# Optimization experiments

Measured on AMD Instinct MI355X. Metric: run time of the kernel, lower is better.

## Reference

```python
import jax, jax.numpy as jnp
import numpy as np

B, T, D, NH, V, L = 2, 1024, 1024, 16, 32000, 4  # L = blocks * layers_per_block
HD = D // NH
FF = 4 * D


def rmsnorm(x, gamma, beta):
    # matches RMSNorm: mean of squares over last dim (tp pmean is identity on 1 device)
    ms = jnp.mean(jnp.square(x), axis=-1, keepdims=True)
    return (x / jnp.sqrt(ms + 1e-6)) * gamma + beta


def setup_inputs() -> dict:
    key = jax.random.key(0)
    ks = jax.random.split(key, 16)
    s = 0.02
    inp = {
        "tokens": jax.random.randint(ks[0], (B, T), 0, V, dtype=jnp.int32),
        "emb_W": jax.random.normal(ks[1], (V, D), jnp.float32) * s,
        "pos_W": jax.random.normal(ks[2], (T, D), jnp.float32) * s,
        "g1": jnp.ones((L, D), jnp.float32),
        "be1": jnp.zeros((L, D), jnp.float32),
        "Wqkv": jax.random.normal(ks[3], (L, D, 3 * D), jnp.float32) * s,
        "bqkv": jnp.zeros((L, 3 * D), jnp.float32),
        "Wo": jax.random.normal(ks[4], (L, D, D), jnp.float32) * s,
        "bo": jnp.zeros((L, D), jnp.float32),
        "g2": jnp.ones((L, D), jnp.float32),
        "be2": jnp.zeros((L, D), jnp.float32),
        "Wf1": jax.random.normal(ks[5], (L, D, FF), jnp.float32) * s,
        "bf1": jnp.zeros((L, FF), jnp.float32),
        "Wf2": jax.random.normal(ks[6], (L, FF, D), jnp.float32) * s,
        "bf2": jnp.zeros((L, D), jnp.float32),
        "gf": jnp.ones((D,), jnp.float32),
        "bef": jnp.zeros((D,), jnp.float32),
    }
    return inp


def _forward(tokens, emb_W, pos_W, g1, be1, Wqkv, bqkv, Wo, bo, g2, be2,
             Wf1, bf1, Wf2, bf2, gf, bef):
    x = emb_W[tokens] + pos_W[jnp.arange(T)]  # [B, T, D]
    causal = jnp.tril(jnp.ones((T, T), dtype=bool))
    scale = HD ** -0.5
    for i in range(L):
        # attention sub-block
        h = rmsnorm(x, g1[i], be1[i])
        qkv = h @ Wqkv[i] + bqkv[i]
        q, k, v = jnp.split(qkv, 3, axis=-1)
        q = q.reshape(B, T, NH, HD).transpose(0, 2, 1, 3)  # B nh T d
        k = k.reshape(B, T, NH, HD).transpose(0, 2, 1, 3)
        v = v.reshape(B, T, NH, HD).transpose(0, 2, 1, 3)
        att = jnp.einsum('bhqd,bhkd->bhqk', q, k) * scale
        att = jnp.where(causal, att, -jnp.inf)
        att = jax.nn.softmax(att, axis=-1)
        o = jnp.einsum('bhqk,bhkd->bhqd', att, v)
        o = o.transpose(0, 2, 1, 3).reshape(B, T, D)
        x = x + (o @ Wo[i] + bo[i])
        # FFN sub-block (selu, dropout off since train=False)
        h = rmsnorm(x, g2[i], be2[i])
        f = jax.nn.selu(h @ Wf1[i] + bf1[i]) @ Wf2[i] + bf2[i]
        x = x + f
    # tied output head: final RMSNorm then embedding.attend
    x = rmsnorm(x, gf, bef)
    logits = jnp.einsum('btd,vd->btv', x, emb_W)
    return logits


def reference(tokens, emb_W, pos_W, g1, be1, Wqkv, bqkv, Wo, bo, g2, be2,
              Wf1, bf1, Wf2, bf2, gf, bef):
    return _forward(tokens, emb_W, pos_W, g1, be1, Wqkv, bqkv, Wo, bo,
                    g2, be2, Wf1, bf1, Wf2, bf2, gf, bef)
```

## Files before the change

kernel.cpp:

```cpp
#include <hip/hip_runtime.h>

typedef unsigned short u16;
typedef __attribute__((ext_vector_type(8))) short bf16x8;
typedef __attribute__((ext_vector_type(4))) float f32x4;

#define DD 1024
#define TT 1024
#define NHH 16
#define VV 32000
#define FFF 4096
#define LL 4
#define MM 2048
#define TD3 3072

__device__ __forceinline__ u16 f2bfu(float f) {
  unsigned int x = __builtin_bit_cast(unsigned int, f);
  return (u16)((x + 0x7FFFu + ((x >> 16) & 1u)) >> 16);
}

__device__ __forceinline__ void gl16(const u16* g, u16* l) {
  __builtin_amdgcn_global_load_lds((const __attribute__((address_space(1))) void*)g,
                                   (__attribute__((address_space(3))) void*)l, 16, 0, 0);
}

template <int N>
__device__ __forceinline__ void vwait() {
  if constexpr (N == 0) asm volatile("s_waitcnt vmcnt(0)" ::: "memory");
  else if constexpr (N == 4) asm volatile("s_waitcnt vmcnt(4)" ::: "memory");
  else asm volatile("s_waitcnt vmcnt(8)" ::: "memory");
}

__global__ void transpose_cvt_k(const float* __restrict__ in, u16* __restrict__ out,
                                int K, int N) {
  const size_t mat = (size_t)K * N;
  in += (size_t)blockIdx.z * mat;
  out += (size_t)blockIdx.z * mat;
  __shared__ float tile[32][33];
  const int n0 = blockIdx.x << 5, k0 = blockIdx.y << 5;
  const int tx = threadIdx.x, ty = threadIdx.y;
#pragma unroll
  for (int i = 0; i < 32; i += 8) tile[ty + i][tx] = in[(size_t)(k0 + ty + i) * N + n0 + tx];
  __syncthreads();
#pragma unroll
  for (int i = 0; i < 32; i += 8)
    out[(size_t)(n0 + ty + i) * K + k0 + tx] = f2bfu(tile[tx][ty + i]);
}

__global__ void cvt_bf16_k(const float* __restrict__ in, u16* __restrict__ out, long n4) {
  const long i = (long)blockIdx.x * blockDim.x + threadIdx.x;
  if (i >= n4) return;
  const float4 v = ((const float4*)in)[i];
  ushort4 o;
  o.x = f2bfu(v.x); o.y = f2bfu(v.y); o.z = f2bfu(v.z); o.w = f2bfu(v.w);
  ((ushort4*)out)[i] = o;
}

__global__ void embed_k(const int* __restrict__ tok, const float* __restrict__ emb,
                        const float* __restrict__ pos, float* __restrict__ x) {
  const int m = blockIdx.x, tid = threadIdx.x;
  const int t = m & (TT - 1);
  const int id = tok[m];
  const float4 e = ((const float4*)(emb + (size_t)id * DD))[tid];
  const float4 p = ((const float4*)(pos + (size_t)t * DD))[tid];
  float4 r;
  r.x = e.x + p.x; r.y = e.y + p.y; r.z = e.z + p.z; r.w = e.w + p.w;
  ((float4*)(x + (size_t)m * DD))[tid] = r;
}

__global__ void rmsnorm_k(const float* __restrict__ x, const float* __restrict__ g,
                          const float* __restrict__ be, u16* __restrict__ out) {
  const int row = blockIdx.x, tid = threadIdx.x;
  const float4 xv = ((const float4*)(x + (size_t)row * DD))[tid];
  float ss = xv.x * xv.x + xv.y * xv.y + xv.z * xv.z + xv.w * xv.w;
#pragma unroll
  for (int o = 32; o; o >>= 1) ss += __shfl_xor(ss, o);
  __shared__ float sm[4];
  if ((tid & 63) == 0) sm[tid >> 6] = ss;
  __syncthreads();
  const float tot = sm[0] + sm[1] + sm[2] + sm[3];
  const float rs = rsqrtf(tot * (1.f / DD) + 1e-6f);
  const float4 gv = ((const float4*)g)[tid];
  const float4 bv = ((const float4*)be)[tid];
  ushort4 o4;
  o4.x = f2bfu(xv.x * rs * gv.x + bv.x);
  o4.y = f2bfu(xv.y * rs * gv.y + bv.y);
  o4.z = f2bfu(xv.z * rs * gv.z + bv.z);
  o4.w = f2bfu(xv.w * rs * gv.w + bv.w);
  ((ushort4*)(out + (size_t)row * DD))[tid] = o4;
}

template <int NP>
__global__ void addres_rms_k(float* __restrict__ x, const float* __restrict__ pp,
                             const float* __restrict__ bias, const float* __restrict__ g,
                             const float* __restrict__ be, u16* __restrict__ out) {
  const int row = blockIdx.x, tid = threadIdx.x;
  const size_t base = (size_t)row * (DD / 4) + tid;
  float4 s = ((float4*)x)[base];
  const float4 bv = ((const float4*)bias)[tid];
  s.x += bv.x; s.y += bv.y; s.z += bv.z; s.w += bv.w;
#pragma unroll
  for (int p = 0; p < NP; ++p) {
    const float4 pv = ((const float4*)pp)[(size_t)p * (MM * DD / 4) + base];
    s.x += pv.x; s.y += pv.y; s.z += pv.z; s.w += pv.w;
  }
  ((float4*)x)[base] = s;
  float ss = s.x * s.x + s.y * s.y + s.z * s.z + s.w * s.w;
#pragma unroll
  for (int o = 32; o; o >>= 1) ss += __shfl_xor(ss, o);
  __shared__ float sm[4];
  if ((tid & 63) == 0) sm[tid >> 6] = ss;
  __syncthreads();
  const float tot = sm[0] + sm[1] + sm[2] + sm[3];
  const float rs = rsqrtf(tot * (1.f / DD) + 1e-6f);
  const float4 gv = ((const float4*)g)[tid];
  const float4 bev = ((const float4*)be)[tid];
  ushort4 o4;
  o4.x = f2bfu(s.x * rs * gv.x + bev.x);
  o4.y = f2bfu(s.y * rs * gv.y + bev.y);
  o4.z = f2bfu(s.z * rs * gv.z + bev.z);
  o4.w = f2bfu(s.w * rs * gv.w + bev.w);
  ((ushort4*)(out + (size_t)row * DD))[tid] = o4;
}

__global__ void pack_vt_k(const u16* __restrict__ qkv, u16* __restrict__ Vt) {
  const int z = blockIdx.x;
  const int t0 = blockIdx.y << 6;
  const int b = z >> 4, h = z & 15;
  __shared__ u16 tile[64][72];
  const int tid = threadIdx.x;
  for (int c = tid; c < 512; c += 256) {
    const int t = c >> 3, d8 = (c & 7) << 3;
    union { uint4 u; u16 s[8]; } tmp;
    tmp.u = *(const uint4*)(qkv + (long)(b * TT + t0 + t) * TD3 + 2 * DD + h * 64 + d8);
#pragma unroll
    for (int j = 0; j < 8; ++j) tile[d8 + j][t] = tmp.s[j];
  }
  __syncthreads();
  for (int c = tid; c < 512; c += 256) {
    const int d = c >> 3, t8 = (c & 7) << 3;
    *(uint4*)(Vt + ((long)z * 64 + d) * TT + t0 + t8) = *(const uint4*)&tile[d][t8];
  }
}

__global__ __launch_bounds__(256) void flash_k(const u16* __restrict__ qkv,
                                               const u16* __restrict__ Vt,
                                               u16* __restrict__ o) {
  const int z = blockIdx.x;
  const int pair = blockIdx.y;
  const int b = z >> 4, h = z & 15;
  const int tid = threadIdx.x;
  const int lane = tid & 63;
  const int w = tid >> 6;

  __shared__ u16 Qs[64 * 64];
  __shared__ u16 Ks[128 * 64];
  __shared__ u16 Vs[64 * 128];
  __shared__ u16 Ps[64 * 128];

  const u16* qbase = qkv + (size_t)b * TT * TD3;
  const int kcb = (lane >> 4) << 4;

  for (int half = 0; half < 2; ++half) {
    const int qa = half ? (15 - pair) : pair;
    const int q0 = qa << 6;
    const int nkt = (qa >> 1) + 1;

#pragma unroll
    for (int c = 0; c < 2; ++c) {
      const int rbase = c * 32 + w * 8;
      const int row = rbase + (lane >> 3);
      const u16* src = qbase + (long)(q0 + row) * TD3 + h * 64 +
                       ((((lane & 7) << 4) ^ ((row & 7) << 4)) >> 1);
      gl16(src, &Qs[rbase * 64]);
    }

    float m_r[4], l_r[4];
    f32x4 oacc[4];
#pragma unroll
    for (int r = 0; r < 4; ++r) { m_r[r] = -1e30f; l_r[r] = 0.f; }
#pragma unroll
    for (int nd = 0; nd < 4; ++nd) oacc[nd] = (f32x4){0.f, 0.f, 0.f, 0.f};

    for (int kt = 0; kt < nkt; ++kt) {
      const int t0 = kt << 7;
#pragma unroll
      for (int c = 0; c < 4; ++c) {
        const int rbase = c * 32 + w * 8;
        const int row = rbase + (lane >> 3);
        const u16* src = qbase + (long)(t0 + row) * TD3 + DD + h * 64 +
                         ((((lane & 7) << 4) ^ ((row & 7) << 4)) >> 1);
        gl16(src, &Ks[rbase * 64]);
      }
#pragma unroll
      for (int c = 0; c < 4; ++c) {
        const int rbase = c * 16 + w * 4;
        const int d = rbase + (lane >> 4);
        const u16* src = Vt + ((long)(z * 64 + d)) * TT + t0 +
                         ((((lane & 15) << 4) ^ ((d & 7) << 4)) >> 1);
        gl16(src, &Vs[rbase * 128]);
      }
      __syncthreads();

      f32x4 sacc[8];
#pragma unroll
      for (int ni = 0; ni < 8; ++ni) sacc[ni] = (f32x4){0.f, 0.f, 0.f, 0.f};
      const int qrow = (w << 4) + (lane & 15);
#pragma unroll
      for (int ks = 0; ks < 2; ++ks) {
        const bf16x8 aq = *(const bf16x8*)&Qs[qrow * 64 + (((ks * 64 + kcb) ^ ((qrow & 7) << 4)) >> 1)];
#pragma unroll
        for (int ni = 0; ni < 8; ++ni) {
          const int key = (lane & 15) + (ni << 4);
          const bf16x8 bk = *(const bf16x8*)&Ks[key * 64 + (((ks * 64 + kcb) ^ ((key & 7) << 4)) >> 1)];
          sacc[ni] = __builtin_amdgcn_mfma_f32_16x16x32_bf16(aq, bk, sacc[ni], 0, 0, 0);
        }
      }

      float mx[4] = {-1e30f, -1e30f, -1e30f, -1e30f};
      const bool diag = (kt == nkt - 1);
#pragma unroll
      for (int ni = 0; ni < 8; ++ni)
#pragma unroll
        for (int r = 0; r < 4; ++r) {
          float v = sacc[ni][r] * 0.125f;
          if (diag) {
            const int key = t0 + (lane & 15) + (ni << 4);
            const int qq = q0 + (w << 4) + ((lane >> 4) << 2) + r;
            if (key > qq) v = -1e30f;
          }
          sacc[ni][r] = v;
          mx[r] = fmaxf(mx[r], v);
        }
#pragma unroll
      for (int st = 1; st < 16; st <<= 1)
#pragma unroll
        for (int r = 0; r < 4; ++r) mx[r] = fmaxf(mx[r], __shfl_xor(mx[r], st));
      float sc[4], sum[4];
#pragma unroll
      for (int r = 0; r < 4; ++r) {
        const float mn = fmaxf(m_r[r], mx[r]);
        sc[r] = __expf(m_r[r] - mn);
        m_r[r] = mn;
        sum[r] = 0.f;
      }
#pragma unroll
      for (int ni = 0; ni < 8; ++ni)
#pragma unroll
        for (int r = 0; r < 4; ++r) {
          const float e = __expf(sacc[ni][r] - m_r[r]);
          sum[r] += e;
          const int prow = (w << 4) + ((lane >> 4) << 2) + r;
          const int pcol = (lane & 15) + (ni << 4);
          Ps[prow * 128 + (((pcol << 1) ^ ((prow & 7) << 4)) >> 1)] = f2bfu(e);
        }
#pragma unroll
      for (int st = 1; st < 16; st <<= 1)
#pragma unroll
        for (int r = 0; r < 4; ++r) sum[r] += __shfl_xor(sum[r], st);
#pragma unroll
      for (int r = 0; r < 4; ++r) l_r[r] = l_r[r] * sc[r] + sum[r];
#pragma unroll
      for (int nd = 0; nd < 4; ++nd)
#pragma unroll
        for (int r = 0; r < 4; ++r) oacc[nd][r] *= sc[r];

#pragma unroll
      for (int ks2 = 0; ks2 < 4; ++ks2) {
        const int prow = (w << 4) + (lane & 15);
        const bf16x8 pa = *(const bf16x8*)&Ps[prow * 128 + (((ks2 * 64 + kcb) ^ ((prow & 7) << 4)) >> 1)];
#pragma unroll
        for (int nd = 0; nd < 4; ++nd) {
          const int dd2 = (lane & 15) + (nd << 4);
          const bf16x8 vb = *(const bf16x8*)&Vs[dd2 * 128 + (((ks2 * 64 + kcb) ^ ((dd2 & 7) << 4)) >> 1)];
          oacc[nd] = __builtin_amdgcn_mfma_f32_16x16x32_bf16(pa, vb, oacc[nd], 0, 0, 0);
        }
      }
      __syncthreads();
    }

    float inv[4];
#pragma unroll
    for (int r = 0; r < 4; ++r) inv[r] = 1.f / l_r[r];
#pragma unroll
    for (int nd = 0; nd < 4; ++nd)
#pragma unroll
      for (int r = 0; r < 4; ++r) {
        const int row = q0 + (w << 4) + ((lane >> 4) << 2) + r;
        const int col = (h << 6) + (lane & 15) + (nd << 4);
        o[(long)(b * TT + row) * DD + col] = f2bfu(oacc[nd][r] * inv[r]);
      }
  }
}

enum { EPI_BF16 = 0, EPI_BF16_BIAS = 1, EPI_SELU = 2, EPI_F32 = 3, EPI_RESID = 4 };

template <int EPI>
__global__ __launch_bounds__(256) void gemm_bt(
    const u16* __restrict__ A, long az1, long az2, int lda,
    const u16* __restrict__ Bt, long bz1, long bz2, int ldb,
    void* __restrict__ C, long cz1, long cz2, int ldc,
    const float* __restrict__ bias, int Nvalid, int K) {
  const int z = blockIdx.z;
  A += (long)(z >> 4) * az1 + (long)(z & 15) * az2;
  Bt += (long)(z >> 4) * bz1 + (long)(z & 15) * bz2;
  const long coff = (long)(z >> 4) * cz1 + (long)(z & 15) * cz2;

  __shared__ u16 ldsA[2][128 * 32];
  __shared__ u16 ldsB[2][128 * 32];

  const int tid = threadIdx.x;
  const int lane = tid & 63;
  const int wave = tid >> 6;
  const int wr = wave >> 1, wc = wave & 1;
  const int m0 = blockIdx.x << 7, n0 = blockIdx.y << 7;

  f32x4 acc[4][4];
#pragma unroll
  for (int i = 0; i < 4; ++i)
#pragma unroll
    for (int j = 0; j < 4; ++j) acc[i][j] = (f32x4){0.f, 0.f, 0.f, 0.f};

  auto STAGE = [&](int buf, int kt) {
    const int k0 = kt << 5;
#pragma unroll
    for (int p = 0; p < 2; ++p) {
      const int c = tid + (p << 8);
      const int row = c >> 2, col = (c & 3) << 3;
      gl16(A + (long)(m0 + row) * lda + k0 + col, &ldsA[buf][c << 3]);
      gl16(Bt + (long)(n0 + row) * ldb + k0 + col, &ldsB[buf][c << 3]);
    }
  };

  const int nk = K >> 5;
  STAGE(0, 0);
  __syncthreads();
  int cur = 0;
  for (int kt = 0; kt < nk; ++kt) {
    if (kt + 1 < nk) STAGE(cur ^ 1, kt + 1);
    const int rb = lane & 15;
    const int kc = (lane >> 4) << 3;
    bf16x8 af[4], bfr[4];
#pragma unroll
    for (int mi = 0; mi < 4; ++mi)
      af[mi] = *(const bf16x8*)&ldsA[cur][(((wr << 6) + (mi << 4) + rb) << 5) + kc];
#pragma unroll
    for (int ni = 0; ni < 4; ++ni)
      bfr[ni] = *(const bf16x8*)&ldsB[cur][(((wc << 6) + (ni << 4) + rb) << 5) + kc];
#pragma unroll
    for (int mi = 0; mi < 4; ++mi)
#pragma unroll
      for (int ni = 0; ni < 4; ++ni)
        acc[mi][ni] = __builtin_amdgcn_mfma_f32_16x16x32_bf16(af[mi], bfr[ni], acc[mi][ni], 0, 0, 0);
    __syncthreads();
    cur ^= 1;
  }

  const int row0 = m0 + (wr << 6) + ((lane >> 4) << 2);
  const int col0 = n0 + (wc << 6) + (lane & 15);
#pragma unroll
  for (int ni = 0; ni < 4; ++ni) {
    const int col = col0 + (ni << 4);
    if (col >= Nvalid) continue;
    float bv = 0.f;
    if (EPI == EPI_BF16_BIAS || EPI == EPI_SELU || EPI == EPI_RESID) bv = bias[col];
#pragma unroll
    for (int mi = 0; mi < 4; ++mi) {
#pragma unroll
      for (int r = 0; r < 4; ++r) {
        const int row = row0 + (mi << 4) + r;
        const long idx = coff + (long)row * ldc + col;
        float v = acc[mi][ni][r] + bv;
        if (EPI == EPI_SELU)
          v = v > 0.f ? 1.0507009873554805f * v : 1.7580993408473766f * (__expf(v) - 1.f);
        if (EPI == EPI_BF16 || EPI == EPI_BF16_BIAS || EPI == EPI_SELU)
          ((u16*)C)[idx] = f2bfu(v);
        else if (EPI == EPI_F32)
          ((float*)C)[idx] = v;
        else
          ((float*)C)[idx] += v;
      }
    }
  }
}

template <int EPI>
__global__ __launch_bounds__(256) void gemm_bt3(
    const u16* __restrict__ A, long az1, long az2, int lda,
    const u16* __restrict__ Bt, long bz1, long bz2, int ldb,
    void* __restrict__ C, long cz1, long cz2, int ldc,
    const float* __restrict__ bias, int Nvalid, int K) {
  const int z = blockIdx.z;
  A += (long)(z >> 4) * az1 + (long)(z & 15) * az2;
  Bt += (long)(z >> 4) * bz1 + (long)(z & 15) * bz2;
  const long coff = (long)(z >> 4) * cz1 + (long)(z & 15) * cz2;

  __shared__ u16 ldsA[3][128 * 32];
  __shared__ u16 ldsB[3][128 * 32];

  const int tid = threadIdx.x;
  const int lane = tid & 63;
  const int wave = tid >> 6;
  const int wr = wave >> 1, wc = wave & 1;
  const int m0 = blockIdx.x << 7, n0 = blockIdx.y << 7;

  f32x4 acc[4][4];
#pragma unroll
  for (int i = 0; i < 4; ++i)
#pragma unroll
    for (int j = 0; j < 4; ++j) acc[i][j] = (f32x4){0.f, 0.f, 0.f, 0.f};

  auto STAGE = [&](int buf, int kt) {
    const int k0 = kt << 5;
#pragma unroll
    for (int p = 0; p < 2; ++p) {
      const int c = tid + (p << 8);
      const int row = c >> 2, col = (c & 3) << 3;
      gl16(A + (long)(m0 + row) * lda + k0 + col, &ldsA[buf][c << 3]);
      gl16(Bt + (long)(n0 + row) * ldb + k0 + col, &ldsB[buf][c << 3]);
    }
  };

  const int nk = K >> 5;
  STAGE(0, 0);
  STAGE(1, 1);

  const int rb = lane & 15;
  const int kc = (lane >> 4) << 3;
  int cur = 0, stg = 2;
#pragma unroll 1
  for (int kt = 0; kt < nk; ++kt) {
    if (kt + 1 < nk) vwait<4>();
    else vwait<0>();
    __builtin_amdgcn_s_barrier();
    __builtin_amdgcn_sched_barrier(0);

    bf16x8 af[4], bfr[4];
#pragma unroll
    for (int mi = 0; mi < 4; ++mi)
      af[mi] = *(const bf16x8*)&ldsA[cur][(((wr << 6) + (mi << 4) + rb) << 5) + kc];
#pragma unroll
    for (int ni = 0; ni < 4; ++ni)
      bfr[ni] = *(const bf16x8*)&ldsB[cur][(((wc << 6) + (ni << 4) + rb) << 5) + kc];
    asm volatile("s_waitcnt lgkmcnt(0)" ::: "memory");
    __builtin_amdgcn_sched_barrier(0);
    __builtin_amdgcn_s_barrier();
    __builtin_amdgcn_sched_barrier(0);
    if (kt + 2 < nk) STAGE(stg, kt + 2);
    __builtin_amdgcn_sched_barrier(0);

    __builtin_amdgcn_s_setprio(1);
#pragma unroll
    for (int mi = 0; mi < 4; ++mi)
#pragma unroll
      for (int ni = 0; ni < 4; ++ni)
        acc[mi][ni] = __builtin_amdgcn_mfma_f32_16x16x32_bf16(af[mi], bfr[ni], acc[mi][ni], 0, 0, 0);
    __builtin_amdgcn_s_setprio(0);

    cur = (cur == 2) ? 0 : cur + 1;
    stg = (stg == 2) ? 0 : stg + 1;
  }

  const int row0 = m0 + (wr << 6) + ((lane >> 4) << 2);
  const int col0 = n0 + (wc << 6) + (lane & 15);
#pragma unroll
  for (int ni = 0; ni < 4; ++ni) {
    const int col = col0 + (ni << 4);
    if (col >= Nvalid) continue;
    float bv = 0.f;
    if (EPI == EPI_BF16_BIAS || EPI == EPI_SELU || EPI == EPI_RESID) bv = bias[col];
#pragma unroll
    for (int mi = 0; mi < 4; ++mi) {
#pragma unroll
      for (int r = 0; r < 4; ++r) {
        const int row = row0 + (mi << 4) + r;
        const long idx = coff + (long)row * ldc + col;
        float v = acc[mi][ni][r] + bv;
        if (EPI == EPI_SELU)
          v = v > 0.f ? 1.0507009873554805f * v : 1.7580993408473766f * (__expf(v) - 1.f);
        if (EPI == EPI_BF16 || EPI == EPI_BF16_BIAS || EPI == EPI_SELU)
          ((u16*)C)[idx] = f2bfu(v);
        else if (EPI == EPI_F32)
          ((float*)C)[idx] = v;
        else
          ((float*)C)[idx] += v;
      }
    }
  }
}

template <int KDIM>
__global__ __launch_bounds__(512) void gemm256_k(
    const u16* __restrict__ A, int lda,
    const u16* __restrict__ Bt, int ldb,
    float* __restrict__ C, int ldc, int mm) {
  extern __shared__ u16 smem[];
  u16* SA = smem;
  u16* SB = smem + 24576;

  const int nwg = gridDim.x;
  const int q = nwg >> 3, r = nwg & 7;
  const int xcd = blockIdx.x & 7, loc = blockIdx.x >> 3;
  const int wg = (xcd < r) ? (xcd * (q + 1) + loc) : (r * (q + 1) + (xcd - r) * q + loc);
  const int m0 = (wg % mm) << 8;
  const int n0 = (wg / mm) << 8;

  const int tid = threadIdx.x;
  const int lane = tid & 63;
  const int w = tid >> 6;
  const int wr = w >> 2, wc = w & 3;
  const int l = lane & 15, kq = lane >> 4;

  f32x4 acc[8][4];
#pragma unroll
  for (int i = 0; i < 8; ++i)
#pragma unroll
    for (int j = 0; j < 4; ++j) acc[i][j] = (f32x4){0.f, 0.f, 0.f, 0.f};

  auto STAGE = [&](int p, int kt) {
    u16* la = SA + (p << 13);
    u16* lb = SB + (p << 13);
    const int k0 = kt << 5;
#pragma unroll
    for (int hh = 0; hh < 2; ++hh) {
      const int c = tid + (hh << 9);
      const int r2 = c >> 3, sp = c & 7;
      const int s = sp ^ (r2 & 7);
      const int row = r2 + ((s >> 2) << 7);
      const int col = k0 + ((s & 3) << 3);
      gl16(A + (size_t)(m0 + row) * lda + col, la + (c << 3));
      gl16(Bt + (size_t)(n0 + row) * ldb + col, lb + (c << 3));
    }
  };

  constexpr int NK = KDIM >> 5;
  STAGE(0, 0);
  STAGE(1, 1);
  STAGE(2, 2);

  int buf = 0;
#pragma unroll 1
  for (int t = 0; t < NK; ++t) {
    if (t + 2 < NK) vwait<8>();
    else if (t + 1 < NK) vwait<4>();
    else vwait<0>();
    __builtin_amdgcn_s_barrier();
    __builtin_amdgcn_sched_barrier(0);

    const u16* a = SA + (buf << 13);
    const u16* b = SB + (buf << 13);
    auto rdA = [&](int mi) -> bf16x8 {
      const int row = (wr << 7) + (mi << 4) + l;
      const int r2 = row & 127;
      const int sp = (((row >> 7) << 2) + kq) ^ (r2 & 7);
      return *(const bf16x8*)&a[(r2 << 6) + (sp << 3)];
    };
    auto rdB = [&](int ni) -> bf16x8 {
      const int row = (wc << 6) + (ni << 4) + l;
      const int r2 = row & 127;
      const int sp = (((row >> 7) << 2) + kq) ^ (r2 & 7);
      return *(const bf16x8*)&b[(r2 << 6) + (sp << 3)];
    };

    bf16x8 af[8], bfr[4];
#pragma unroll
    for (int ni = 0; ni < 4; ++ni) bfr[ni] = rdB(ni);
#pragma unroll
    for (int mi = 0; mi < 8; ++mi) af[mi] = rdA(mi);
    asm volatile("s_waitcnt lgkmcnt(0)" ::: "memory");
    __builtin_amdgcn_sched_barrier(0);
    __builtin_amdgcn_s_barrier();
    __builtin_amdgcn_sched_barrier(0);
    if (t + 3 < NK) STAGE(buf, t + 3);
    __builtin_amdgcn_sched_barrier(0);

    __builtin_amdgcn_s_setprio(1);
#pragma unroll
    for (int mi = 0; mi < 8; ++mi)
#pragma unroll
      for (int ni = 0; ni < 4; ++ni)
        acc[mi][ni] = __builtin_amdgcn_mfma_f32_16x16x32_bf16(af[mi], bfr[ni], acc[mi][ni], 0, 0, 0);
    __builtin_amdgcn_s_setprio(0);
    buf = (buf == 2) ? 0 : buf + 1;
  }

  float* lf = (float*)smem + (size_t)w * 1088;
#pragma unroll 1
  for (int mi = 0; mi < 8; ++mi) {
    asm volatile("s_waitcnt lgkmcnt(0)" ::: "memory");
    __builtin_amdgcn_sched_barrier(0);
#pragma unroll
    for (int ni = 0; ni < 4; ++ni)
#pragma unroll
      for (int rr = 0; rr < 4; ++rr)
        lf[((kq << 2) + rr) * 68 + (ni << 4) + l] = acc[mi][ni][rr];
    asm volatile("s_waitcnt lgkmcnt(0)" ::: "memory");
    __builtin_amdgcn_sched_barrier(0);
#pragma unroll
    for (int p = 0; p < 4; ++p) {
      const int rl = (p << 2) + kq;
      const f32x4 v = *(const f32x4*)&lf[rl * 68 + (l << 2)];
      const int row = m0 + (wr << 7) + (mi << 4) + rl;
      const int col = n0 + (wc << 6) + (l << 2);
      *(f32x4*)(C + (size_t)row * ldc + col) = v;
    }
  }
}

extern "C" void kernel_launch(void* const* d_in, const int* in_sizes, int n_in,
                              void* d_out, int out_size, void* d_ws, size_t ws_size,
                              hipStream_t stream) {
  const int* tokens = (const int*)d_in[0];
  const float* emb_W = (const float*)d_in[1];
  const float* pos_W = (const float*)d_in[2];
  const float* g1 = (const float*)d_in[3];
  const float* be1 = (const float*)d_in[4];
  const float* Wqkv = (const float*)d_in[5];
  const float* bqkv = (const float*)d_in[6];
  const float* Wo = (const float*)d_in[7];
  const float* bo = (const float*)d_in[8];
  const float* g2 = (const float*)d_in[9];
  const float* be2 = (const float*)d_in[10];
  const float* Wf1 = (const float*)d_in[11];
  const float* bf1 = (const float*)d_in[12];
  const float* Wf2 = (const float*)d_in[13];
  const float* bf2 = (const float*)d_in[14];
  const float* gf = (const float*)d_in[15];
  const float* bef = (const float*)d_in[16];

  char* w = (char*)d_ws;
  auto alloc = [&](size_t bytes) {
    char* p = w;
    w += (bytes + 255) & ~(size_t)255;
    return p;
  };
  u16* WqkvT = (u16*)alloc((size_t)LL * TD3 * DD * 2);
  u16* WoT   = (u16*)alloc((size_t)LL * DD * DD * 2);
  u16* Wf1T  = (u16*)alloc((size_t)LL * FFF * DD * 2);
  u16* Wf2T  = (u16*)alloc((size_t)LL * DD * FFF * 2);
  u16* embB  = (u16*)alloc((size_t)VV * DD * 2);
  float* x   = (float*)alloc((size_t)MM * DD * 4);
  u16* h     = (u16*)alloc((size_t)MM * DD * 2);
  u16* qkv   = (u16*)alloc((size_t)MM * TD3 * 2);
  u16* Vt    = (u16*)alloc((size_t)32 * 64 * TT * 2);
  u16* o     = (u16*)alloc((size_t)MM * DD * 2);
  u16* h1    = (u16*)alloc((size_t)MM * FFF * 2);
  float* pp  = (float*)alloc((size_t)4 * MM * DD * 4);

  bool big =
      hipFuncSetAttribute((const void*)&gemm256_k<1024>,
                          hipFuncAttributeMaxDynamicSharedMemorySize, 98304) == hipSuccess;

  dim3 tb(32, 8);
  transpose_cvt_k<<<dim3(TD3 / 32, DD / 32, LL), tb, 0, stream>>>(Wqkv, WqkvT, DD, TD3);
  transpose_cvt_k<<<dim3(DD / 32, DD / 32, LL), tb, 0, stream>>>(Wo, WoT, DD, DD);
  transpose_cvt_k<<<dim3(FFF / 32, DD / 32, LL), tb, 0, stream>>>(Wf1, Wf1T, DD, FFF);
  transpose_cvt_k<<<dim3(DD / 32, FFF / 32, LL), tb, 0, stream>>>(Wf2, Wf2T, FFF, DD);
  cvt_bf16_k<<<(VV * DD / 4) / 256, 256, 0, stream>>>(emb_W, embB, (long)VV * DD / 4);
  embed_k<<<MM, 256, 0, stream>>>(tokens, emb_W, pos_W, x);
  rmsnorm_k<<<MM, 256, 0, stream>>>(x, g1, be1, h);

  for (int i = 0; i < LL; ++i) {
    gemm_bt3<EPI_BF16_BIAS><<<dim3(16, 24, 1), 256, 0, stream>>>(
        h, 0, 0, DD, WqkvT + (size_t)i * TD3 * DD, 0, 0, DD,
        qkv, 0, 0, TD3, bqkv + i * TD3, TD3, DD);
    pack_vt_k<<<dim3(32, 16), 256, 0, stream>>>(qkv, Vt);
    flash_k<<<dim3(32, 8), 256, 0, stream>>>(qkv, Vt, o);
    gemm_bt3<EPI_F32><<<dim3(16, 8, 2), 256, 0, stream>>>(
        o, 0, 512, DD, WoT + (size_t)i * DD * DD, 0, 512, DD,
        pp, 0, (long)MM * DD, DD, nullptr, DD, 512);
    addres_rms_k<2><<<MM, 256, 0, stream>>>(x, pp, bo + i * DD, g2 + i * DD, be2 + i * DD, h);
    gemm_bt3<EPI_SELU><<<dim3(16, 32, 1), 256, 0, stream>>>(
        h, 0, 0, DD, Wf1T + (size_t)i * FFF * DD, 0, 0, DD,
        h1, 0, 0, FFF, bf1 + i * FFF, FFF, DD);
    gemm_bt3<EPI_F32><<<dim3(16, 8, 4), 256, 0, stream>>>(
        h1, 0, 1024, FFF, Wf2T + (size_t)i * DD * FFF, 0, 1024, FFF,
        pp, 0, (long)MM * DD, DD, nullptr, DD, 1024);
    const bool last = (i == LL - 1);
    addres_rms_k<4><<<MM, 256, 0, stream>>>(
        x, pp, bf2 + i * DD,
        last ? gf : g1 + (i + 1) * DD, last ? bef : be1 + (i + 1) * DD, h);
  }

  if (big) {
    gemm256_k<1024><<<1000, 512, 98304, stream>>>(
        h, DD, embB, DD, (float*)d_out, VV, 8);
  } else {
    gemm_bt<EPI_F32><<<dim3(16, 250, 1), 256, 0, stream>>>(
        h, 0, 0, DD, embB, 0, 0, DD,
        (float*)d_out, 0, 0, VV, nullptr, VV, DD);
  }
}
```

Measured before the change: 1.064 ms.

## Interleave LDS fragment reads with MFMA groups and store epilogue directly

Result: faster. 959.2 us (-9.9%).

```diff
diff --git a/kernel.cpp b/kernel.cpp
--- a/kernel.cpp
+++ b/kernel.cpp
@@ -488,11 +488,12 @@
   }
 }
 
-template <int KDIM>
+template <int EPI, int KDIM>
 __global__ __launch_bounds__(512) void gemm256_k(
     const u16* __restrict__ A, int lda,
     const u16* __restrict__ Bt, int ldb,
-    float* __restrict__ C, int ldc, int mm) {
+    void* __restrict__ C, int ldc,
+    const float* __restrict__ bias, int mm) {
   extern __shared__ u16 smem[];
   u16* SA = smem;
   u16* SB = smem + 24576;
@@ -561,11 +562,42 @@
       return *(const bf16x8*)&b[(r2 << 6) + (sp << 3)];
     };
 
-    bf16x8 af[8], bfr[4];
-#pragma unroll
-    for (int ni = 0; ni < 4; ++ni) bfr[ni] = rdB(ni);
-#pragma unroll
-    for (int mi = 0; mi < 8; ++mi) af[mi] = rdA(mi);
+    bf16x8 bfr[4], afA[2], afB[2];
+    bfr[0] = rdB(0); bfr[1] = rdB(1); bfr[2] = rdB(2); bfr[3] = rdB(3);
+    afA[0] = rdA(0); afA[1] = rdA(1);
+    __builtin_amdgcn_sched_barrier(0);
+    afB[0] = rdA(2); afB[1] = rdA(3);
+    __builtin_amdgcn_sched_barrier(0);
+
+    __builtin_amdgcn_s_setprio(1);
+#pragma unroll
+    for (int ni = 0; ni < 4; ++ni) {
+      acc[0][ni] = __builtin_amdgcn_mfma_f32_16x16x32_bf16(afA[0], bfr[ni], acc[0][ni], 0, 0, 0);
+      acc[1][ni] = __builtin_amdgcn_mfma_f32_16x16x32_bf16(afA[1], bfr[ni], acc[1][ni], 0, 0, 0);
+    }
+    __builtin_amdgcn_s_setprio(0);
+    __builtin_amdgcn_sched_barrier(0);
+    afA[0] = rdA(4); afA[1] = rdA(5);
+    __builtin_amdgcn_sched_barrier(0);
+    __builtin_amdgcn_s_setprio(1);
+#pragma unroll
+    for (int ni = 0; ni < 4; ++ni) {
+      acc[2][ni] = __builtin_amdgcn_mfma_f32_16x16x32_bf16(afB[0], bfr[ni], acc[2][ni], 0, 0, 0);
+      acc[3][ni] = __builtin_amdgcn_mfma_f32_16x16x32_bf16(afB[1], bfr[ni], acc[3][ni], 0, 0, 0);
+    }
+    __builtin_amdgcn_s_setprio(0);
+    __builtin_amdgcn_sched_barrier(0);
+    afB[0] = rdA(6); afB[1] = rdA(7);
+    __builtin_amdgcn_sched_barrier(0);
+    __builtin_amdgcn_s_setprio(1);
+#pragma unroll
+    for (int ni = 0; ni < 4; ++ni) {
+      acc[4][ni] = __builtin_amdgcn_mfma_f32_16x16x32_bf16(afA[0], bfr[ni], acc[4][ni], 0, 0, 0);
+      acc[5][ni] = __builtin_amdgcn_mfma_f32_16x16x32_bf16(afA[1], bfr[ni], acc[5][ni], 0, 0, 0);
+    }
+    __builtin_amdgcn_s_setprio(0);
+    __builtin_amdgcn_sched_barrier(0);
+
     asm volatile("s_waitcnt lgkmcnt(0)" ::: "memory");
     __builtin_amdgcn_sched_barrier(0);
     __builtin_amdgcn_s_barrier();
@@ -575,33 +607,35 @@
 
     __builtin_amdgcn_s_setprio(1);
 #pragma unroll
-    for (int mi = 0; mi < 8; ++mi)
-#pragma unroll
-      for (int ni = 0; ni < 4; ++ni)
-        acc[mi][ni] = __builtin_amdgcn_mfma_f32_16x16x32_bf16(af[mi], bfr[ni], acc[mi][ni], 0, 0, 0);
+    for (int ni = 0; ni < 4; ++ni) {
+      acc[6][ni] = __builtin_amdgcn_mfma_f32_16x16x32_bf16(afB[0], bfr[ni], acc[6][ni], 0, 0, 0);
+      acc[7][ni] = __builtin_amdgcn_mfma_f32_16x16x32_bf16(afB[1], bfr[ni], acc[7][ni], 0, 0, 0);
+    }
     __builtin_amdgcn_s_setprio(0);
     buf = (buf == 2) ? 0 : buf + 1;
   }
 
-  float* lf = (float*)smem + (size_t)w * 1088;
-#pragma unroll 1
-  for (int mi = 0; mi < 8; ++mi) {
-    asm volatile("s_waitcnt lgkmcnt(0)" ::: "memory");
-    __builtin_amdgcn_sched_barrier(0);
-#pragma unroll
-    for (int ni = 0; ni < 4; ++ni)
-#pragma unroll
-      for (int rr = 0; rr < 4; ++rr)
-        lf[((kq << 2) + rr) * 68 + (ni << 4) + l] = acc[mi][ni][rr];
-    asm volatile("s_waitcnt lgkmcnt(0)" ::: "memory");
-    __builtin_amdgcn_sched_barrier(0);
-#pragma unroll
-    for (int p = 0; p < 4; ++p) {
-      const int rl = (p << 2) + kq;
-      const f32x4 v = *(const f32x4*)&lf[rl * 68 + (l << 2)];
-      const int row = m0 + (wr << 7) + (mi << 4) + rl;
-      const int col = n0 + (wc << 6) + (l << 2);
-      *(f32x4*)(C + (size_t)row * ldc + col) = v;
+  const int row0 = m0 + (wr << 7) + ((lane >> 4) << 2);
+  const int col0 = n0 + (wc << 6) + (lane & 15);
+#pragma unroll
+  for (int ni = 0; ni < 4; ++ni) {
+    const int col = col0 + (ni << 4);
+    float bv = 0.f;
+    if (EPI == EPI_BF16_BIAS || EPI == EPI_SELU) bv = bias[col];
+#pragma unroll
+    for (int mi = 0; mi < 8; ++mi) {
+#pragma unroll
+      for (int r = 0; r < 4; ++r) {
+        const int row = row0 + (mi << 4) + r;
+        const long idx = (long)row * ldc + col;
+        float v = acc[mi][ni][r] + bv;
+        if (EPI == EPI_SELU)
+          v = v > 0.f ? 1.0507009873554805f * v : 1.7580993408473766f * (__expf(v) - 1.f);
+        if (EPI == EPI_BF16 || EPI == EPI_BF16_BIAS || EPI == EPI_SELU)
+          ((u16*)C)[idx] = f2bfu(v);
+        else
+          ((float*)C)[idx] = v;
+      }
     }
   }
 }
@@ -647,7 +681,7 @@
   float* pp  = (float*)alloc((size_t)4 * MM * DD * 4);
 
   bool big =
-      hipFuncSetAttribute((const void*)&gemm256_k<1024>,
+      hipFuncSetAttribute((const void*)&gemm256_k<EPI_F32, 1024>,
                           hipFuncAttributeMaxDynamicSharedMemorySize, 98304) == hipSuccess;
 
   dim3 tb(32, 8);
@@ -682,8 +716,8 @@
   }
 
   if (big) {
-    gemm256_k<1024><<<1000, 512, 98304, stream>>>(
-        h, DD, embB, DD, (float*)d_out, VV, 8);
+    gemm256_k<EPI_F32, 1024><<<1000, 512, 98304, stream>>>(
+        h, DD, embB, DD, (float*)d_out, VV, nullptr, 8);
   } else {
     gemm_bt<EPI_F32><<<dim3(16, 250, 1), 256, 0, stream>>>(
         h, 0, 0, DD, embB, 0, 0, DD,
```
